# Optimization experiments

Measured on AMD Instinct MI355X. Metric: run time of the kernel, lower is better.

The kernel has to match this reference:

```python
import jax, jax.numpy as jnp
import numpy as np

EPS = 1e-8  # torch F.cosine_similarity denominator clamp
NEG = -1e9

def setup_inputs() -> dict:
    key = jax.random.key(0)
    k1, k2, k3 = jax.random.split(key, 3)
    B, H, L, D = 16, 16, 4096, 128
    query = jax.random.normal(k1, (B, H, 1, D), dtype=jnp.float32)
    key_t = jax.random.normal(k2, (B, H, L, D), dtype=jnp.float32)
    mask = jax.random.randint(k3, (B, L), 0, 2, dtype=jnp.int32)
    return {"query": query, "key": key_t, "mask": mask}

def reference(query, key, mask):
    # cosine similarity without materializing the repeated query:
    # scores[b,h,l] = <q[b,h,0],k[b,h,l]> / max(||q||*||k||, eps)
    dots = jnp.einsum('bhod,bhld->bhl', query, key)  # o == 1, [B,H,L]
    qn = jnp.linalg.norm(query, axis=3)              # [B,H,1]
    kn = jnp.linalg.norm(key, axis=3)                # [B,H,L]
    scores = dots / jnp.maximum(qn * kn, EPS)        # [B,H,L]
    m = mask[:, None, :]                              # [B,1,L] broadcast over H
    scores = jnp.where(m == 0, NEG, scores)
    p_attn = jax.nn.softmax(scores, axis=2)
    return p_attn
```

## Files before the change

### kernel.cpp

```cpp
#include <hip/hip_runtime.h>
#include <hip/hip_bf16.h>


constexpr int Bdim = 16, Hdim = 16, Ldim = 4096, Ddim = 128;
constexpr int NTHREADS = 1024;
constexpr float EPSF = 1e-8f;
constexpr float NEGF = -1000000000.0f;

__device__ __forceinline__ float dpp_sum32(float v) {
    v += __int_as_float(__builtin_amdgcn_update_dpp(0, __float_as_int(v), 0x111, 0xf, 0xf, true));
    v += __int_as_float(__builtin_amdgcn_update_dpp(0, __float_as_int(v), 0x112, 0xf, 0xf, true));
    v += __int_as_float(__builtin_amdgcn_update_dpp(0, __float_as_int(v), 0x114, 0xf, 0xf, true));
    v += __int_as_float(__builtin_amdgcn_update_dpp(0, __float_as_int(v), 0x118, 0xf, 0xf, true));
    v += __int_as_float(__builtin_amdgcn_update_dpp(0, __float_as_int(v), 0x142, 0xa, 0xf, true));
    return v;
}

__global__ __launch_bounds__(NTHREADS, 8) void attn_cos_softmax(
    const float* __restrict__ q,
    const float* __restrict__ k,
    const int* __restrict__ mask,
    float* __restrict__ out)
{
    const int bh = blockIdx.x;
    const int b  = bh >> 4;
    const float4* qrow = reinterpret_cast<const float4*>(q + (size_t)bh * Ddim);
    const float4* krow = reinterpret_cast<const float4*>(k + (size_t)bh * Ldim * Ddim);
    const int*    mrow = mask + (size_t)b * Ldim;
    float*        orow = out  + (size_t)bh * Ldim;

    __shared__ float s_scores[Ldim];
    __shared__ float s_red[16];

    const int tid  = threadIdx.x;
    const int g    = tid >> 5;
    const int lane = tid & 31;
    const bool writer = (lane == 31);

    float4 qv = qrow[lane];
    float q2 = qv.x*qv.x + qv.y*qv.y + qv.z*qv.z + qv.w*qv.w;
    q2 = dpp_sum32(q2);
    const float qn = sqrtf(q2);

    constexpr int UNROLL = 8;
    constexpr int ROWS_PER_ITER = 32 * UNROLL;
    #pragma unroll 1
    for (int iter = 0; iter < Ldim / ROWS_PER_ITER; ++iter) {
        const int base = iter * ROWS_PER_ITER + g;
        float4 kv[UNROLL];
        #pragma unroll
        for (int j = 0; j < UNROLL; ++j) {
            kv[j] = krow[(base + j * 32) * (Ddim / 4) + lane];
        }
        #pragma unroll
        for (int j = 0; j < UNROLL; ++j) {
            float dp = kv[j].x*qv.x + kv[j].y*qv.y + kv[j].z*qv.z + kv[j].w*qv.w;
            float k2 = kv[j].x*kv[j].x + kv[j].y*kv[j].y + kv[j].z*kv[j].z + kv[j].w*kv[j].w;
            dp = dpp_sum32(dp);
            k2 = dpp_sum32(k2);
            if (writer) {
                float denom = fmaxf(qn * sqrtf(k2), EPSF);
                s_scores[base + j * 32] = dp / denom;
            }
        }
    }
    __syncthreads();

    float sv[4];
    float lmax = -3.0e9f;
    #pragma unroll
    for (int i = 0; i < 4; ++i) {
        const int idx = tid + i * NTHREADS;
        float s = s_scores[idx];
        s = (mrow[idx] == 0) ? NEGF : s;
        sv[i] = s;
        lmax = fmaxf(lmax, s);
    }
    #pragma unroll
    for (int m = 32; m >= 1; m >>= 1) lmax = fmaxf(lmax, __shfl_xor(lmax, m));
    if ((tid & 63) == 0) s_red[tid >> 6] = lmax;
    __syncthreads();
    float gmax = s_red[0];
    #pragma unroll
    for (int i = 1; i < 16; ++i) gmax = fmaxf(gmax, s_red[i]);
    __syncthreads();

    float lsum = 0.0f;
    #pragma unroll
    for (int i = 0; i < 4; ++i) {
        sv[i] = __expf(sv[i] - gmax);
        lsum += sv[i];
    }
    #pragma unroll
    for (int m = 32; m >= 1; m >>= 1) lsum += __shfl_xor(lsum, m);
    if ((tid & 63) == 0) s_red[tid >> 6] = lsum;
    __syncthreads();
    float gsum = 0.0f;
    #pragma unroll
    for (int i = 0; i < 16; ++i) gsum += s_red[i];
    const float rinv = 1.0f / gsum;

    #pragma unroll
    for (int i = 0; i < 4; ++i) {
        orow[tid + i * NTHREADS] = sv[i] * rinv;
    }
}

extern "C" void kernel_launch(void* const* d_in, const int* in_sizes, int n_in,
                              void* d_out, int out_size, void* d_ws, size_t ws_size,
                              hipStream_t stream) {
    const float* q    = (const float*)d_in[0];
    const float* k    = (const float*)d_in[1];
    const int*   mask = (const int*)d_in[2];
    float*       out  = (float*)d_out;

    dim3 grid(Bdim * Hdim);
    dim3 block(NTHREADS);
    attn_cos_softmax<<<grid, block, 0, stream>>>(q, k, mask, out);
}
```

Measured before the change: 97.79 us.

## Fuse mask and online softmax statistics into the score loop

Preloads the mask row into shared memory, applies it while computing each cosine score, and keeps a running max and rescaled sum per 32-lane group (online softmax). After one barrier, the per-group stats are merged and each output is normalized directly. This removes the separate max and sum block reductions and their extra barriers. In exchange the writer lanes do serial exponentials inside the memory-bound load loop and the kernel uses more shared memory.

After: 99.30 us. No clear change (+1.5%).

```diff
diff --git a/kernel.cpp b/kernel.cpp
--- a/kernel.cpp
+++ b/kernel.cpp
@@ -30,17 +30,26 @@
     float*        orow = out  + (size_t)bh * Ldim;
 
     __shared__ float s_scores[Ldim];
-    __shared__ float s_red[16];
+    __shared__ int   s_mask[Ldim];
+    __shared__ float s_m[32];
+    __shared__ float s_z[32];
 
     const int tid  = threadIdx.x;
     const int g    = tid >> 5;
     const int lane = tid & 31;
     const bool writer = (lane == 31);
 
+    reinterpret_cast<int4*>(s_mask)[tid] = reinterpret_cast<const int4*>(mrow)[tid];
+
     float4 qv = qrow[lane];
     float q2 = qv.x*qv.x + qv.y*qv.y + qv.z*qv.z + qv.w*qv.w;
     q2 = dpp_sum32(q2);
     const float qn = sqrtf(q2);
+
+    __syncthreads();
+
+    float m_g = -3.0e9f;
+    float z_g = 0.0f;
 
     constexpr int UNROLL = 8;
     constexpr int ROWS_PER_ITER = 32 * UNROLL;
@@ -59,50 +68,32 @@
             dp = dpp_sum32(dp);
             k2 = dpp_sum32(k2);
             if (writer) {
+                const int row = base + j * 32;
                 float denom = fmaxf(qn * sqrtf(k2), EPSF);
-                s_scores[base + j * 32] = dp / denom;
+                float s = dp / denom;
+                s = (s_mask[row] == 0) ? NEGF : s;
+                s_scores[row] = s;
+                float mn = fmaxf(m_g, s);
+                z_g = z_g * __expf(m_g - mn) + __expf(s - mn);
+                m_g = mn;
             }
         }
     }
+    if (writer) { s_m[g] = m_g; s_z[g] = z_g; }
     __syncthreads();
 
-    float sv[4];
-    float lmax = -3.0e9f;
+    float gmax = s_m[0];
+    #pragma unroll
+    for (int i = 1; i < 32; ++i) gmax = fmaxf(gmax, s_m[i]);
+    float gz = 0.0f;
+    #pragma unroll
+    for (int i = 0; i < 32; ++i) gz += s_z[i] * __expf(s_m[i] - gmax);
+    const float rinv = 1.0f / gz;
+
     #pragma unroll
     for (int i = 0; i < 4; ++i) {
         const int idx = tid + i * NTHREADS;
-        float s = s_scores[idx];
-        s = (mrow[idx] == 0) ? NEGF : s;
-        sv[i] = s;
-        lmax = fmaxf(lmax, s);
-    }
-    #pragma unroll
-    for (int m = 32; m >= 1; m >>= 1) lmax = fmaxf(lmax, __shfl_xor(lmax, m));
-    if ((tid & 63) == 0) s_red[tid >> 6] = lmax;
-    __syncthreads();
-    float gmax = s_red[0];
-    #pragma unroll
-    for (int i = 1; i < 16; ++i) gmax = fmaxf(gmax, s_red[i]);
-    __syncthreads();
-
-    float lsum = 0.0f;
-    #pragma unroll
-    for (int i = 0; i < 4; ++i) {
-        sv[i] = __expf(sv[i] - gmax);
-        lsum += sv[i];
-    }
-    #pragma unroll
-    for (int m = 32; m >= 1; m >>= 1) lsum += __shfl_xor(lsum, m);
-    if ((tid & 63) == 0) s_red[tid >> 6] = lsum;
-    __syncthreads();
-    float gsum = 0.0f;
-    #pragma unroll
-    for (int i = 0; i < 16; ++i) gsum += s_red[i];
-    const float rinv = 1.0f / gsum;
-
-    #pragma unroll
-    for (int i = 0; i < 4; ++i) {
-        orow[tid + i * NTHREADS] = sv[i] * rinv;
+        orow[idx] = __expf(s_scores[idx] - gmax) * rinv;
     }
 }
 
```
